# Kernel tuning notes

Hardware: AMD Instinct MI355X
Metric: run time of the kernel (lower is better)

Reference implementation:

```python
import jax, jax.numpy as jnp
import numpy as np

B, N, D, F_IN, F_OUT, MAX_DEG = 256, 512, 6, 128, 128, 6


def setup_inputs() -> dict:
    key = jax.random.key(0)
    k_atoms, k_deg, k_idx, k_w, k_b = jax.random.split(key, 5)
    atoms = jax.random.normal(k_atoms, (B, N, F_IN), dtype=jnp.float32)
    # structured edges: per-atom degree in [0, MAX_DEG-1], valid neighbor ids in
    # the first `deg` slots, -1 padding afterwards (NGFP convention)
    deg = jax.random.randint(k_deg, (B, N, 1), 0, MAX_DEG)
    nbr = jax.random.randint(k_idx, (B, N, D), 0, N)
    slot = jnp.arange(D)[None, None, :]
    edges = jnp.where(slot < deg, nbr, -1).astype(jnp.int64)
    W = jax.random.normal(k_w, (MAX_DEG, F_IN, F_OUT), dtype=jnp.float32) * (1.0 / np.sqrt(F_IN))
    b = jax.random.normal(k_b, (MAX_DEG, F_OUT), dtype=jnp.float32) * 0.01
    return {"atoms": atoms, "edges": edges, "W": W, "b": b}


def reference(atoms, edges, W, b):
    # lookup_neighbors with include_self=True: gather neighbor rows (-1 -> zero row)
    atoms_p = jnp.pad(atoms, ((0, 0), (1, 0), (0, 0)))          # [B, N+1, F]; row 0 is zeros
    gathered = jax.vmap(lambda a, e: a[e])(atoms_p, edges + 1)  # [B, N, D, F]
    summed = gathered.sum(axis=-2) + atoms                      # [B, N, F] (self included)
    degrees = (edges != -1).sum(axis=-1, keepdims=True)         # [B, N, 1]
    out = jnp.zeros(summed.shape[:-1] + (W.shape[-1],), dtype=summed.dtype)
    for d in range(MAX_DEG):
        h = jax.nn.relu(summed @ W[d] + b[d])                   # [B, N, F_OUT]
        out = out + h * (degrees == d).astype(summed.dtype)
    return out
```

## Files before the change

kernel.cpp:

```cpp
#include <hip/hip_runtime.h>


typedef short bf16x8 __attribute__((ext_vector_type(8)));
typedef float f32x4  __attribute__((ext_vector_type(4)));
typedef unsigned short ushort_t;
typedef unsigned int uint_t;

constexpr int Nn = 512;
constexpr int Ff = 128;

constexpr size_t WS_NEEDED = 196608;

#define BAR_LDS() asm volatile("s_waitcnt lgkmcnt(0)\ns_barrier" ::: "memory")

__device__ inline ushort_t f2bf(float f) {
    uint_t u = __float_as_uint(f);
    return (ushort_t)((u + 0x7FFFu + ((u >> 16) & 1u)) >> 16);
}

__device__ inline bool detect_is64(const int* edges32) {
    int probe = edges32[2 * (threadIdx.x & 63) + 1];
    return __any(probe > 0) == 0;
}

__global__ __launch_bounds__(1024)
void k0_wt(const float* __restrict__ W, ushort_t* __restrict__ Wt) {
    __shared__ float w[128 * 133];
    const int d = blockIdx.x;
    const float* src = W + (size_t)d * 16384;
    #pragma unroll
    for (int i = 0; i < 16; i++) {
        int idx = threadIdx.x + i * 1024;
        w[(idx >> 7) * 133 + (idx & 127)] = src[idx];
    }
    __syncthreads();
    ushort_t* dst = Wt + (size_t)d * 16384;
    #pragma unroll
    for (int i = 0; i < 16; i++) {
        int idx = threadIdx.x + i * 1024;
        dst[idx] = f2bf(w[(idx & 127) * 133 + (idx >> 7)]);
    }
}

__global__ __launch_bounds__(1024, 4)
void k_fused(const float* __restrict__ atoms,
             const int*   __restrict__ edges32,
             const ushort_t* __restrict__ Wt,
             const float* __restrict__ bias,
             float* __restrict__ out) {
    const int tid = threadIdx.x;
    const int mol = blockIdx.x;
    const bool is64 = detect_is64(edges32);

    __shared__ ushort_t summed[Nn * 136];
    __shared__ float4   abuf4[Nn * 2];
    __shared__ ushort_t rlist[Nn];
    __shared__ int hist[6], base_sh[8];

    const float4* gsrc = (const float4*)(atoms + (size_t)mol * (Nn * Ff));
    const int arow = tid >> 1, ac = tid & 1;
    float4 pfA = gsrc[arow * 32 + 0 * 2 + ac];
    float4 pfB = gsrc[arow * 32 + 1 * 2 + ac];

    if (tid < 6) hist[tid] = 0;
    __syncthreads();
    int deg = 0, rk = 0;
    if (tid < Nn) {
        const size_t eb = (size_t)mol * (Nn * 6) + (size_t)tid * 6;
        #pragma unroll
        for (int j = 0; j < 6; j++) {
            int e = is64 ? edges32[(eb + j) * 2] : edges32[eb + j];
            deg += (e >= 0) ? 1 : 0;
        }
        if (deg > 5) deg = 5;
        rk = atomicAdd(&hist[deg], 1);
    }
    __syncthreads();
    if (tid == 0) {
        int a = 0;
        #pragma unroll
        for (int d = 0; d < 6; d++) { base_sh[d] = a; a += hist[d]; }
    }
    __syncthreads();
    if (tid < Nn) rlist[base_sh[deg] + rk] = (ushort_t)tid;
    abuf4[2 * arow + (ac ^ (arow & 1))] = pfA;
    pfA = gsrc[arow * 32 + 2 * 2 + ac];
    BAR_LDS();

    const int pr = tid >> 1, h = tid & 1;
    const int R = rlist[pr];
    int er[6];
    if (is64) {
        const uint4* ep = (const uint4*)(edges32 + ((size_t)mol * (Nn * 6) + (size_t)R * 6) * 2);
        uint4 q0 = ep[0], q1 = ep[1], q2 = ep[2];
        er[0] = (int)q0.x; er[1] = (int)q0.z;
        er[2] = (int)q1.x; er[3] = (int)q1.z;
        er[4] = (int)q2.x; er[5] = (int)q2.z;
    } else {
        const int* ep = edges32 + (size_t)mol * (Nn * 6) + (size_t)R * 6;
        #pragma unroll
        for (int j = 0; j < 6; j++) er[j] = ep[j];
    }
    const int selfb = 2 * R + (h ^ (R & 1));
    const int pubb  = 2 * arow + (ac ^ (arow & 1));

    for (int i = 0; i < 8; i++) {
        const int s0 = 2 * i;
        {
            float4 a = abuf4[selfb];
            #pragma unroll
            for (int j = 0; j < 6; j++) {
                int e = er[j];
                if (e >= 0) {
                    float4 v = abuf4[2 * e + (h ^ (e & 1))];
                    a.x += v.x; a.y += v.y; a.z += v.z; a.w += v.w;
                }
            }
            uint2 o;
            o.x = (uint_t)f2bf(a.x) | ((uint_t)f2bf(a.y) << 16);
            o.y = (uint_t)f2bf(a.z) | ((uint_t)f2bf(a.w) << 16);
            *(uint2*)&summed[R * 136 + s0 * 8 + h * 4] = o;
        }
        BAR_LDS();
        abuf4[pubb] = pfB;
        if (i < 7) pfB = gsrc[arow * 32 + (2 * i + 3) * 2 + ac];
        BAR_LDS();
        {
            float4 a = abuf4[selfb];
            #pragma unroll
            for (int j = 0; j < 6; j++) {
                int e = er[j];
                if (e >= 0) {
                    float4 v = abuf4[2 * e + (h ^ (e & 1))];
                    a.x += v.x; a.y += v.y; a.z += v.z; a.w += v.w;
                }
            }
            uint2 o;
            o.x = (uint_t)f2bf(a.x) | ((uint_t)f2bf(a.y) << 16);
            o.y = (uint_t)f2bf(a.z) | ((uint_t)f2bf(a.w) << 16);
            *(uint2*)&summed[R * 136 + (s0 + 1) * 8 + h * 4] = o;
        }
        if (i < 7) {
            BAR_LDS();
            abuf4[pubb] = pfA;
            if (i < 6) pfA = gsrc[arow * 32 + (2 * i + 4) * 2 + ac];
            BAR_LDS();
        }
    }
    BAR_LDS();

    const int lane = tid & 63, wid = tid >> 6;
    const int kq = lane >> 4, ml = lane & 15;

    int cnts[6], cbase[6], Tp[7];
    {
        int a = 0, b = 0;
        #pragma unroll
        for (int d = 0; d < 6; d++) {
            cnts[d] = hist[d];
            cbase[d] = b; b += cnts[d];
            Tp[d] = a; a += ((cnts[d] + 15) >> 4) * 4;
        }
        Tp[6] = a;
    }
    const int items = Tp[6];

    for (int it = wid; it < items; it += 16) {
        int d = 0;
        #pragma unroll
        for (int dd = 1; dd < 6; dd++) if (it >= Tp[dd]) d = dd;
        const int loc = it - Tp[d];
        const int ti = loc >> 2, ci = loc & 3;
        const int cn = cnts[d], cb = cbase[d];

        int lidx = ti * 16 + ml;
        int cl = (lidx < cn) ? lidx : cn - 1;
        int row = rlist[cb + cl];
        bf16x8 af[4];
        #pragma unroll
        for (int k0 = 0; k0 < 4; k0++)
            af[k0] = *(const bf16x8*)&summed[row * 136 + kq * 8 + k0 * 32];
        int orw[4];
        #pragma unroll
        for (int r = 0; r < 4; r++) {
            int li = ti * 16 + kq * 4 + r;
            orw[r] = (li < cn) ? (int)rlist[cb + li] : -1;
        }
        const ushort_t* wg = Wt + (size_t)d * 16384;
        #pragma unroll
        for (int n2 = 0; n2 < 2; n2++) {
            const int nt = ci * 2 + n2;
            bf16x8 bfr[4];
            #pragma unroll
            for (int k0 = 0; k0 < 4; k0++)
                bfr[k0] = *(const bf16x8*)&wg[(nt * 16 + ml) * 128 + k0 * 32 + kq * 8];
            f32x4 c = {0.f, 0.f, 0.f, 0.f};
            #pragma unroll
            for (int k0 = 0; k0 < 4; k0++)
                c = __builtin_amdgcn_mfma_f32_16x16x32_bf16(af[k0], bfr[k0], c, 0, 0, 0);
            const int col = nt * 16 + ml;
            const float bc = bias[d * Ff + col];
            #pragma unroll
            for (int r = 0; r < 4; r++) {
                if (orw[r] >= 0) {
                    float v = c[r] + bc;
                    out[((size_t)mol * Nn + orw[r]) * Ff + col] = v > 0.f ? v : 0.f;
                }
            }
        }
    }
}

__global__ __launch_bounds__(128, 2)
void graphconv_fallback(const float* __restrict__ atoms,
                        const int* __restrict__ edges_raw,
                        const float* __restrict__ W,
                        const float* __restrict__ bias,
                        float* __restrict__ out) {
    const int tid = threadIdx.x;
    const int d = blockIdx.x % 6;
    const int k = blockIdx.x / 6;
    const int a0 = k * 256;
    __shared__ int eds[256 * 6];
    __shared__ int list[256];
    __shared__ int cnt;
    __shared__ float sv[2][Ff];
    bool is64;
    { int v = edges_raw[2 * (tid & 63) + 1]; is64 = (__ballot(v > 0) == 0ull); }
    if (!is64) { for (int i = tid; i < 256 * 6; i += 128) eds[i] = edges_raw[a0 * 6 + i]; }
    else       { for (int i = tid; i < 256 * 6; i += 128) eds[i] = edges_raw[2 * (a0 * 6 + i)]; }
    if (tid == 0) cnt = 0;
    __syncthreads();
    for (int i = tid; i < 256; i += 128) {
        int deg = 0;
        #pragma unroll
        for (int j = 0; j < 6; j++) deg += (eds[i * 6 + j] != -1) ? 1 : 0;
        if (deg == d) { int p = atomicAdd(&cnt, 1); list[p] = i; }
    }
    float Wreg[Ff];
    { const float* Wd = W + (size_t)d * Ff * Ff;
      #pragma unroll
      for (int f = 0; f < Ff; f++) Wreg[f] = Wd[f * Ff + tid]; }
    const float breg = bias[d * Ff + tid];
    __syncthreads();
    const int n = cnt;
    const float* batch_atoms = atoms + (size_t)(a0 / Nn) * Nn * Ff;
    const int row0 = a0 % Nn;
    for (int ii = 0; ii < n; ii++) {
        const int i = list[ii];
        float s = batch_atoms[(row0 + i) * Ff + tid];
        #pragma unroll
        for (int j = 0; j < 6; j++) {
            int e = eds[i * 6 + j];
            if (e != -1) s += batch_atoms[e * Ff + tid];
        }
        float* buf = sv[ii & 1];
        buf[tid] = s;
        __syncthreads();
        float acc = breg;
        const float4* sv4 = (const float4*)buf;
        #pragma unroll
        for (int fc = 0; fc < Ff / 4; fc++) {
            float4 x = sv4[fc];
            acc = fmaf(x.x, Wreg[4 * fc + 0], acc);
            acc = fmaf(x.y, Wreg[4 * fc + 1], acc);
            acc = fmaf(x.z, Wreg[4 * fc + 2], acc);
            acc = fmaf(x.w, Wreg[4 * fc + 3], acc);
        }
        out[(size_t)(a0 + i) * Ff + tid] = fmaxf(acc, 0.0f);
    }
}

extern "C" void kernel_launch(void* const* d_in, const int* in_sizes, int n_in,
                              void* d_out, int out_size, void* d_ws, size_t ws_size,
                              hipStream_t stream) {
    const float* atoms = (const float*)d_in[0];
    const int*   edges = (const int*)d_in[1];
    const float* W     = (const float*)d_in[2];
    const float* bias  = (const float*)d_in[3];
    float*       outp  = (float*)d_out;

    if (ws_size >= WS_NEEDED) {
        ushort_t* Wt = (ushort_t*)d_ws;
        k0_wt<<<6, 1024, 0, stream>>>(W, Wt);
        k_fused<<<256, 1024, 0, stream>>>(atoms, edges, Wt, bias, outp);
    } else {
        graphconv_fallback<<<3072, 128, 0, stream>>>(atoms, edges, W, bias, outp);
    }
}
```

Measured before the change: 155.2 us.

## Split each molecule across two blocks and swizzle the summed LDS layout

The fused kernel now launches two 512-thread blocks per molecule. Each block computes summed features and the MFMA output for half of the atoms, but still stages the whole molecule's atom rows in LDS for the neighbor gather. The summed buffer switches from padded rows to a k-chunk-major layout with an XOR swizzle, which shrinks LDS use enough to fit more blocks per CU. The degree histogram and row list now alias into existing LDS buffers. In exchange, every atom row is loaded from global memory twice, and each block issues more loads per thread.

```diff
diff --git a/kernel.cpp b/kernel.cpp
--- a/kernel.cpp
+++ b/kernel.cpp
@@ -42,130 +42,128 @@
     }
 }
 
-__global__ __launch_bounds__(1024, 4)
+__global__ __launch_bounds__(512, 4)
 void k_fused(const float* __restrict__ atoms,
              const int*   __restrict__ edges32,
              const ushort_t* __restrict__ Wt,
              const float* __restrict__ bias,
              float* __restrict__ out) {
-    const int tid = threadIdx.x;
-    const int mol = blockIdx.x;
+    const int tid  = threadIdx.x;
+    const int mol  = blockIdx.x & 255;
+    const int half = blockIdx.x >> 8;
+    const int r0   = half * 256;
     const bool is64 = detect_is64(edges32);
 
-    __shared__ ushort_t summed[Nn * 136];
-    __shared__ float4   abuf4[Nn * 2];
-    __shared__ ushort_t rlist[Nn];
-    __shared__ int hist[6], base_sh[8];
+    __shared__ __attribute__((aligned(16))) ushort_t summed[32768];
+    __shared__ float4 abuf4[1024];
+    int*      hist  = (int*)&summed[32752];
+    ushort_t* rlist = (ushort_t*)abuf4;
 
     const float4* gsrc = (const float4*)(atoms + (size_t)mol * (Nn * Ff));
-    const int arow = tid >> 1, ac = tid & 1;
-    float4 pfA = gsrc[arow * 32 + 0 * 2 + ac];
-    float4 pfB = gsrc[arow * 32 + 1 * 2 + ac];
+    const int pr = tid >> 1, h = tid & 1;
+    const int arow0 = pr, arow1 = pr + 256;
+    float4 pfA0 = gsrc[arow0 * 32 + 0 * 2 + h];
+    float4 pfA1 = gsrc[arow1 * 32 + 0 * 2 + h];
+    float4 pfB0 = gsrc[arow0 * 32 + 1 * 2 + h];
+    float4 pfB1 = gsrc[arow1 * 32 + 1 * 2 + h];
 
     if (tid < 6) hist[tid] = 0;
-    __syncthreads();
-    int deg = 0, rk = 0;
-    if (tid < Nn) {
-        const size_t eb = (size_t)mol * (Nn * 6) + (size_t)tid * 6;
-        #pragma unroll
-        for (int j = 0; j < 6; j++) {
-            int e = is64 ? edges32[(eb + j) * 2] : edges32[eb + j];
-            deg += (e >= 0) ? 1 : 0;
-        }
-        if (deg > 5) deg = 5;
-        rk = atomicAdd(&hist[deg], 1);
-    }
-    __syncthreads();
-    if (tid == 0) {
-        int a = 0;
-        #pragma unroll
-        for (int d = 0; d < 6; d++) { base_sh[d] = a; a += hist[d]; }
-    }
-    __syncthreads();
-    if (tid < Nn) rlist[base_sh[deg] + rk] = (ushort_t)tid;
-    abuf4[2 * arow + (ac ^ (arow & 1))] = pfA;
-    pfA = gsrc[arow * 32 + 2 * 2 + ac];
-    BAR_LDS();
-
-    const int pr = tid >> 1, h = tid & 1;
-    const int R = rlist[pr];
+    const int Rg = r0 + pr;
     int er[6];
     if (is64) {
-        const uint4* ep = (const uint4*)(edges32 + ((size_t)mol * (Nn * 6) + (size_t)R * 6) * 2);
+        const uint4* ep = (const uint4*)(edges32 + ((size_t)mol * (Nn * 6) + (size_t)Rg * 6) * 2);
         uint4 q0 = ep[0], q1 = ep[1], q2 = ep[2];
         er[0] = (int)q0.x; er[1] = (int)q0.z;
         er[2] = (int)q1.x; er[3] = (int)q1.z;
         er[4] = (int)q2.x; er[5] = (int)q2.z;
     } else {
-        const int* ep = edges32 + (size_t)mol * (Nn * 6) + (size_t)R * 6;
-        #pragma unroll
-        for (int j = 0; j < 6; j++) er[j] = ep[j];
-    }
-    const int selfb = 2 * R + (h ^ (R & 1));
-    const int pubb  = 2 * arow + (ac ^ (arow & 1));
+        const uint2* ep = (const uint2*)(edges32 + (size_t)mol * (Nn * 6) + (size_t)Rg * 6);
+        uint2 q0 = ep[0], q1 = ep[1], q2 = ep[2];
+        er[0] = (int)q0.x; er[1] = (int)q0.y;
+        er[2] = (int)q1.x; er[3] = (int)q1.y;
+        er[4] = (int)q2.x; er[5] = (int)q2.y;
+    }
+    int deg = 0;
+    #pragma unroll
+    for (int j = 0; j < 6; j++) deg += (er[j] >= 0) ? 1 : 0;
+    if (deg > 5) deg = 5;
+    BAR_LDS();
+    int rk = 0;
+    if (h == 0) rk = atomicAdd(&hist[deg], 1);
+    BAR_LDS();
+    int cnts[6], cbase[6];
+    {
+        int a = 0;
+        #pragma unroll
+        for (int d = 0; d < 6; d++) { cnts[d] = hist[d]; cbase[d] = a; a += cnts[d]; }
+    }
+    abuf4[2 * arow0 + (h ^ (arow0 & 1))] = pfA0;
+    abuf4[2 * arow1 + (h ^ (arow1 & 1))] = pfA1;
+    pfA0 = gsrc[arow0 * 32 + 2 * 2 + h];
+    pfA1 = gsrc[arow1 * 32 + 2 * 2 + h];
+    BAR_LDS();
+
+    const int selfb = 2 * Rg + (h ^ (Rg & 1));
+    const int pubb0 = 2 * arow0 + (h ^ (arow0 & 1));
+    const int pubb1 = 2 * arow1 + (h ^ (arow1 & 1));
+
+#define GATHER(S) do {                                                          \
+        float4 a_ = abuf4[selfb];                                               \
+        _Pragma("unroll")                                                       \
+        for (int j_ = 0; j_ < 6; j_++) {                                        \
+            int e_ = er[j_];                                                    \
+            if (e_ >= 0) {                                                      \
+                float4 v_ = abuf4[2 * e_ + (h ^ (e_ & 1))];                     \
+                a_.x += v_.x; a_.y += v_.y; a_.z += v_.z; a_.w += v_.w;         \
+            }                                                                   \
+        }                                                                       \
+        const int g_ = ((S) >> 2) * 1024 + pr * 4 + (((S) & 3) ^ (pr & 3));     \
+        uint2 o_;                                                               \
+        o_.x = (uint_t)f2bf(a_.x) | ((uint_t)f2bf(a_.y) << 16);                 \
+        o_.y = (uint_t)f2bf(a_.z) | ((uint_t)f2bf(a_.w) << 16);                 \
+        *(uint2*)&summed[g_ * 8 + h * 4] = o_;                                  \
+    } while (0)
 
     for (int i = 0; i < 8; i++) {
-        const int s0 = 2 * i;
-        {
-            float4 a = abuf4[selfb];
-            #pragma unroll
-            for (int j = 0; j < 6; j++) {
-                int e = er[j];
-                if (e >= 0) {
-                    float4 v = abuf4[2 * e + (h ^ (e & 1))];
-                    a.x += v.x; a.y += v.y; a.z += v.z; a.w += v.w;
-                }
-            }
-            uint2 o;
-            o.x = (uint_t)f2bf(a.x) | ((uint_t)f2bf(a.y) << 16);
-            o.y = (uint_t)f2bf(a.z) | ((uint_t)f2bf(a.w) << 16);
-            *(uint2*)&summed[R * 136 + s0 * 8 + h * 4] = o;
-        }
+        GATHER(2 * i);
         BAR_LDS();
-        abuf4[pubb] = pfB;
-        if (i < 7) pfB = gsrc[arow * 32 + (2 * i + 3) * 2 + ac];
+        abuf4[pubb0] = pfB0;
+        abuf4[pubb1] = pfB1;
+        if (i < 7) {
+            pfB0 = gsrc[arow0 * 32 + (2 * i + 3) * 2 + h];
+            pfB1 = gsrc[arow1 * 32 + (2 * i + 3) * 2 + h];
+        }
         BAR_LDS();
-        {
-            float4 a = abuf4[selfb];
-            #pragma unroll
-            for (int j = 0; j < 6; j++) {
-                int e = er[j];
-                if (e >= 0) {
-                    float4 v = abuf4[2 * e + (h ^ (e & 1))];
-                    a.x += v.x; a.y += v.y; a.z += v.z; a.w += v.w;
-                }
-            }
-            uint2 o;
-            o.x = (uint_t)f2bf(a.x) | ((uint_t)f2bf(a.y) << 16);
-            o.y = (uint_t)f2bf(a.z) | ((uint_t)f2bf(a.w) << 16);
-            *(uint2*)&summed[R * 136 + (s0 + 1) * 8 + h * 4] = o;
-        }
+        GATHER(2 * i + 1);
         if (i < 7) {
             BAR_LDS();
-            abuf4[pubb] = pfA;
-            if (i < 6) pfA = gsrc[arow * 32 + (2 * i + 4) * 2 + ac];
+            abuf4[pubb0] = pfA0;
+            abuf4[pubb1] = pfA1;
+            if (i < 6) {
+                pfA0 = gsrc[arow0 * 32 + (2 * i + 4) * 2 + h];
+                pfA1 = gsrc[arow1 * 32 + (2 * i + 4) * 2 + h];
+            }
             BAR_LDS();
         }
     }
+#undef GATHER
+    BAR_LDS();
+    if (h == 0) rlist[cbase[deg] + rk] = (ushort_t)pr;
     BAR_LDS();
 
     const int lane = tid & 63, wid = tid >> 6;
     const int kq = lane >> 4, ml = lane & 15;
 
-    int cnts[6], cbase[6], Tp[7];
+    int Tp[7];
     {
-        int a = 0, b = 0;
-        #pragma unroll
-        for (int d = 0; d < 6; d++) {
-            cnts[d] = hist[d];
-            cbase[d] = b; b += cnts[d];
-            Tp[d] = a; a += ((cnts[d] + 15) >> 4) * 4;
-        }
+        int a = 0;
+        #pragma unroll
+        for (int d = 0; d < 6; d++) { Tp[d] = a; a += ((cnts[d] + 15) >> 4) * 4; }
         Tp[6] = a;
     }
     const int items = Tp[6];
 
-    for (int it = wid; it < items; it += 16) {
+    for (int it = wid; it < items; it += 8) {
         int d = 0;
         #pragma unroll
         for (int dd = 1; dd < 6; dd++) if (it >= Tp[dd]) d = dd;
@@ -179,7 +177,7 @@
         bf16x8 af[4];
         #pragma unroll
         for (int k0 = 0; k0 < 4; k0++)
-            af[k0] = *(const bf16x8*)&summed[row * 136 + kq * 8 + k0 * 32];
+            af[k0] = *(const bf16x8*)&summed[(k0 * 1024 + row * 4 + (kq ^ (row & 3))) * 8];
         int orw[4];
         #pragma unroll
         for (int r = 0; r < 4; r++) {
@@ -204,7 +202,7 @@
             for (int r = 0; r < 4; r++) {
                 if (orw[r] >= 0) {
                     float v = c[r] + bc;
-                    out[((size_t)mol * Nn + orw[r]) * Ff + col] = v > 0.f ? v : 0.f;
+                    out[((size_t)mol * Nn + r0 + orw[r]) * Ff + col] = v > 0.f ? v : 0.f;
                 }
             }
         }
@@ -283,7 +281,7 @@
     if (ws_size >= WS_NEEDED) {
         ushort_t* Wt = (ushort_t*)d_ws;
         k0_wt<<<6, 1024, 0, stream>>>(W, Wt);
-        k_fused<<<256, 1024, 0, stream>>>(atoms, edges, Wt, bias, outp);
+        k_fused<<<512, 512, 0, stream>>>(atoms, edges, Wt, bias, outp);
     } else {
         graphconv_fallback<<<3072, 128, 0, stream>>>(atoms, edges, W, bias, outp);
     }
```

Result: slower. 163.4 us (+5.3%).
